# Kernel tuning notes

Measured on AMD Instinct MI355X. Metric: run time of the kernel, lower is better.

## Reference

```python
import jax, jax.numpy as jnp
import numpy as np

LN_EPS = 1e-5


def conv2d(x, w, b, stride, pad):
    # x: NCHW, w: OIHW
    y = jax.lax.conv_general_dilated(
        x, w, (stride, stride), [(pad, pad), (pad, pad)],
        dimension_numbers=("NCHW", "OIHW", "NCHW"))
    return y + b[None, :, None, None]


def gdn(x, gamma, beta):
    # y_c = x_c / sqrt(beta_c + sum_j gamma_cj * x_j^2)  (1x1 conv on x^2)
    norm = jnp.einsum("bchw,dc->bdhw", x * x, gamma) + beta[None, :, None, None]
    return x / jnp.sqrt(norm)


def layernorm(x, w, b):
    mu = jnp.mean(x, axis=-1, keepdims=True)
    var = jnp.var(x, axis=-1, keepdims=True)
    return (x - mu) / jnp.sqrt(var + LN_EPS) * w + b


def setup_inputs() -> dict:
    key = jax.random.key(0)
    ks = jax.random.split(key, 16)
    r = lambda i, shape: (jax.random.normal(ks[i], shape) * 0.02).astype(jnp.float32)
    N, M, K, D = 128, 192, 192, 128
    return {
        "x_p": jax.random.normal(ks[0], (4, 16, 3, 64, 64), jnp.float32),
        "y_g": jax.random.normal(ks[1], (64, K, 32), jnp.float32),
        "conv1_w": r(2, (N, 3, 5, 5)), "conv1_b": jnp.zeros((N,), jnp.float32),
        "gamma1": (0.1 * jnp.eye(N) + 1e-3).astype(jnp.float32), "beta1": jnp.ones((N,), jnp.float32),
        "conv2_w": r(3, (N, N, 5, 5)), "conv2_b": jnp.zeros((N,), jnp.float32),
        "gamma2": (0.1 * jnp.eye(N) + 1e-3).astype(jnp.float32), "beta2": jnp.ones((N,), jnp.float32),
        "conv3_w": r(4, (M, N, 3, 3)), "conv3_b": jnp.zeros((M,), jnp.float32),
        "ln_q_w": jnp.ones((M,), jnp.float32), "ln_q_b": jnp.zeros((M,), jnp.float32),
        "ln_kv_w": jnp.ones((K,), jnp.float32), "ln_kv_b": jnp.zeros((K,), jnp.float32),
        "ln_out_w": jnp.ones((M,), jnp.float32), "ln_out_b": jnp.zeros((M,), jnp.float32),
        "Wq": r(5, (D, M)), "Wk": r(6, (D, K)), "v_w": r(7, (1, D)),
        "Wv": r(8, (M, K)), "out_w": r(9, (M, M)), "out_b": jnp.zeros((M,), jnp.float32),
    }


def reference(x_p, y_g, conv1_w, conv1_b, gamma1, beta1, conv2_w, conv2_b,
              gamma2, beta2, conv3_w, conv3_b, ln_q_w, ln_q_b, ln_kv_w, ln_kv_b,
              ln_out_w, ln_out_b, Wq, Wk, v_w, Wv, out_w, out_b):
    B, P, C, Hp, Wp = x_p.shape
    x = x_p.reshape(B * P, C, Hp, Wp)
    # local encoder: conv s2 -> GDN -> conv s2 -> GDN -> conv s1 k3
    x = gdn(conv2d(x, conv1_w, conv1_b, 2, 2), gamma1, beta1)
    x = gdn(conv2d(x, conv2_w, conv2_b, 2, 2), gamma2, beta2)
    y_local = conv2d(x, conv3_w, conv3_b, 1, 1)          # (BP, M, h, w)
    BP, M, h, w = y_local.shape
    q = y_local.reshape(BP, M, h * w).transpose(0, 2, 1)  # (BP, Tq, M)
    kv = y_g.reshape(BP, y_g.shape[1], -1).transpose(0, 2, 1)  # (BP, Tk, K)
    q = layernorm(q, ln_q_w, ln_q_b)
    kv = layernorm(kv, ln_kv_w, ln_kv_b)
    # Bahdanau additive attention
    q_proj = jnp.einsum("bqm,dm->bqd", q, Wq)            # (BP, Tq, D)
    k_proj = jnp.einsum("bkc,dc->bkd", kv, Wk)           # (BP, Tk, D)
    energy = jnp.einsum("bqkd,d->bqk",
                        jnp.tanh(q_proj[:, :, None, :] + k_proj[:, None, :, :]),
                        v_w[0])                           # (BP, Tq, Tk)
    alpha = jax.nn.softmax(energy, axis=-1)
    v_proj = jnp.einsum("bkc,mc->bkm", kv, Wv)           # (BP, Tk, M)
    context = jnp.einsum("bqk,bkm->bqm", alpha, v_proj)
    context = jnp.einsum("bqm,nm->bqn", context, out_w) + out_b
    fused = layernorm(q + context, ln_out_w, ln_out_b)
    return fused.transpose(0, 2, 1).reshape(BP, M, h, w)
```

## Files before the change

### kernel.cpp

```cpp
#include <hip/hip_runtime.h>
#include <cstddef>
#include <cstdint>


typedef __bf16 bf16x8 __attribute__((ext_vector_type(8)));
typedef float floatx4 __attribute__((ext_vector_type(4)));
typedef unsigned short ushortT;
typedef unsigned short ushort8v __attribute__((ext_vector_type(8)));

#if __has_builtin(__builtin_amdgcn_exp2f)
#define EXP2F(x) __builtin_amdgcn_exp2f(x)
#else
#define EXP2F(x) exp2f(x)
#endif
#if __has_builtin(__builtin_amdgcn_rcpf)
#define RCPF(x) __builtin_amdgcn_rcpf(x)
#else
#define RCPF(x) (1.f / (x))
#endif

__device__ __forceinline__ ushortT f2bf(float f) {
  unsigned u = __builtin_bit_cast(unsigned, f);
  unsigned r = (u + 0x7FFFu + ((u >> 16) & 1u)) >> 16;
  return (ushortT)r;
}
__device__ __forceinline__ float bf2f(ushortT u) {
  return __builtin_bit_cast(float, ((unsigned)u) << 16);
}

static constexpr size_t OFF_X2BF = 4194304;
static constexpr size_t OFF_X3BF = 9437184;
static constexpr size_t OFF_QRAW = 10485760;
static constexpr size_t OFF_WBQ  = 21299200;
static constexpr size_t OFF_WBK  = 21311488;
static constexpr size_t OFF_WBV  = 21323776;
static constexpr size_t OFF_WBO  = 21342208;
static constexpr size_t OFF_WT2  = 26079232;
static constexpr size_t OFF_WT3  = 26284032;
static constexpr size_t OFF_WC1  = 26394624;
static constexpr size_t OFF_GB1  = 26406912;
static constexpr size_t OFF_GB2  = 26415104;
static constexpr size_t OFF_KP   = 0;
static constexpr size_t OFF_VT   = 262144;

__device__ __constant__ int d_TWI2[4][9] = {{ 0, 2, 4,10,12,14,20,22,24},
                                            { 1, 3,11,13,21,23, 0, 0, 0},
                                            { 5, 7, 9,15,17,19, 0, 0, 0},
                                            { 6, 8,16,18, 0, 0, 0, 0, 0}};
__device__ __constant__ int d_NT2[4] = {9, 6, 6, 4};

__device__ void dev_convw3_v8(const float* w, ushortT* wt, int mode, int idx8,
                              int total8) {
  if (idx8 >= total8) return;
  int base = idx8 << 3;
  int om   = (base >> 3) & 63;
  int kg   = (base >> 9) & 3;
  int slab = base >> 11;
  int mt, s, tap, T;
  if (mode == 0) {
    int ph;
    if (slab < 72) ph = 0; else if (slab < 120) ph = 1;
    else if (slab < 168) ph = 2; else ph = 3;
    const int st[4] = {0, 72, 120, 168};
    const int ns[4] = {36, 24, 24, 16};
    int rel = slab - st[ph];
    mt = rel / ns[ph]; s = rel % ns[ph];
    tap = d_TWI2[ph][s >> 2]; T = 25;
  } else {
    mt = slab / 36; s = slab % 36; tap = s >> 2; T = 9;
  }
  int cc = s & 3;
  int c0 = cc * 32 + kg * 8;
  int oc = mt * 64 + om;
  const float* wp = w + (size_t)(oc * 128 + c0) * T + tap;
  ushort8v o;
  #pragma unroll
  for (int j = 0; j < 8; ++j) o[j] = f2bf(wp[(size_t)j * T]);
  *(ushort8v*)&wt[base] = o;
}

__device__ void dev_convw1_v8(const float* w, ushortT* wt, int idx8) {
  if (idx8 >= 2560) return;
  int base = idx8 << 3;
  int k0   = base & 31;
  int oc   = (base >> 5) & 127;
  int slab = base >> 12;
  int ph, i;
  if (slab < 2) { ph = 0; i = slab; } else { ph = slab - 1; i = 0; }
  int kg = k0 >> 3;
  ushort8v o;
  #pragma unroll
  for (int jj = 0; jj < 8; ++jj) {
    int tidx = i * 8 + jj;
    float val = 0.f;
    if (kg < 3 && tidx < d_NT2[ph]) {
      int tap = d_TWI2[ph][tidx];
      val = w[(size_t)(oc * 3 + kg) * 25 + tap];
    }
    o[jj] = f2bf(val);
  }
  *(ushort8v*)&wt[base] = o;
}

__device__ void dev_wcast_v8(const float* w, ushortT* wb, int total8,
                             float scale, int idx8) {
  if (idx8 >= total8) return;
  int base = idx8 << 3;
  float4 a = *(const float4*)&w[base];
  float4 c = *(const float4*)&w[base + 4];
  ushort8v o;
  o[0] = f2bf(a.x * scale); o[1] = f2bf(a.y * scale);
  o[2] = f2bf(a.z * scale); o[3] = f2bf(a.w * scale);
  o[4] = f2bf(c.x * scale); o[5] = f2bf(c.y * scale);
  o[6] = f2bf(c.z * scale); o[7] = f2bf(c.w * scale);
  *(ushort8v*)&wb[base] = o;
}

__global__ __launch_bounds__(256) void prep_kernel(
    const float* __restrict__ conv2_w, ushortT* __restrict__ wt2,
    const float* __restrict__ conv3_w, ushortT* __restrict__ wt3,
    const float* __restrict__ conv1_w, ushortT* __restrict__ wc1,
    const float* __restrict__ Wq, ushortT* __restrict__ wbq,
    const float* __restrict__ Wk, ushortT* __restrict__ wbk,
    const float* __restrict__ Wv, ushortT* __restrict__ wbv,
    const float* __restrict__ out_w, ushortT* __restrict__ wbo,
    const float* __restrict__ gamma1, ushortT* __restrict__ gb1,
    const float* __restrict__ gamma2, ushortT* __restrict__ gb2) {
  constexpr float C2LE = 2.88539008177792681f;
  int blk = blockIdx.x, tid = threadIdx.x;
  if (blk < 200)       dev_convw3_v8(conv2_w, wt2, 0, blk * 256 + tid, 51200);
  else if (blk < 308)  dev_convw3_v8(conv3_w, wt3, 1, (blk - 200) * 256 + tid, 27648);
  else if (blk < 318)  dev_convw1_v8(conv1_w, wc1, (blk - 308) * 256 + tid);
  else if (blk < 330)  dev_wcast_v8(Wq, wbq, 3072, C2LE, (blk - 318) * 256 + tid);
  else if (blk < 342)  dev_wcast_v8(Wk, wbk, 3072, C2LE, (blk - 330) * 256 + tid);
  else if (blk < 360)  dev_wcast_v8(Wv, wbv, 4608, 1.f, (blk - 342) * 256 + tid);
  else if (blk < 378)  dev_wcast_v8(out_w, wbo, 4608, 1.f, (blk - 360) * 256 + tid);
  else if (blk < 386)  dev_wcast_v8(gamma1, gb1, 2048, 1.f, (blk - 378) * 256 + tid);
  else                 dev_wcast_v8(gamma2, gb2, 2048, 1.f, (blk - 386) * 256 + tid);
}

__global__ __launch_bounds__(256, 2) void conv1_kv_kernel(
    const float* __restrict__ x, const ushortT* __restrict__ wc1,
    const float* __restrict__ bias, const ushortT* __restrict__ gb1,
    const float* __restrict__ beta1, ushortT* __restrict__ outb,
    const float* __restrict__ yg, const float* __restrict__ ln_kv_w,
    const float* __restrict__ ln_kv_b, const ushortT* __restrict__ wbk,
    const ushortT* __restrict__ wbv, float* __restrict__ kp,
    ushortT* __restrict__ vT) {
  __shared__ ushortT smem[28416];
  int tid  = threadIdx.x;
  int wave = tid >> 6;
  int lane = tid & 63;
  int ln15 = lane & 15;
  int kg   = lane >> 4;

  if (blockIdx.x >= 512) {
    int b = blockIdx.x - 512;
    float*   skvRaw = (float*)smem;
    ushortT* skv    = smem + 12416;

    const float4* yg4 = (const float4*)(yg + (size_t)b * 6144);
    for (int j = tid; j < 1536; j += 256) {
      float4 v = yg4[j];
      int c = j >> 3;
      int t4 = (j & 7) * 4;
      skvRaw[(t4 + 0) * 194 + c] = v.x;
      skvRaw[(t4 + 1) * 194 + c] = v.y;
      skvRaw[(t4 + 2) * 194 + c] = v.z;
      skvRaw[(t4 + 3) * 194 + c] = v.w;
    }
    __syncthreads();
    for (int r = wave; r < 32; r += 4) {
      const float* src = skvRaw + r * 194;
      float v0 = src[lane], v1 = src[lane + 64], v2 = src[lane + 128];
      float s = v0 + v1 + v2;
      float s2 = v0 * v0 + v1 * v1 + v2 * v2;
      #pragma unroll
      for (int off = 32; off; off >>= 1) { s += __shfl_xor(s, off); s2 += __shfl_xor(s2, off); }
      float mean = s * (1.f / 192.f);
      float var = s2 * (1.f / 192.f) - mean * mean;
      float inv = rsqrtf(var + 1e-5f);
      skv[r * 200 + lane]       = f2bf((v0 - mean) * inv * ln_kv_w[lane]       + ln_kv_b[lane]);
      skv[r * 200 + lane + 64]  = f2bf((v1 - mean) * inv * ln_kv_w[lane + 64]  + ln_kv_b[lane + 64]);
      skv[r * 200 + lane + 128] = f2bf((v2 - mean) * inv * ln_kv_w[lane + 128] + ln_kv_b[lane + 128]);
    }
    __syncthreads();
    for (int ti = wave; ti < 40; ti += 4) {
      floatx4 acc = (floatx4)0.f;
      if (ti < 16) {
        int rt = ti >> 3, ct = ti & 7;
        #pragma unroll
        for (int k0 = 0; k0 < 192; k0 += 32) {
          bf16x8 afr = *(const bf16x8*)&skv[(rt * 16 + ln15) * 200 + k0 + kg * 8];
          bf16x8 bfr = *(const bf16x8*)&wbk[((size_t)(ct * 16 + ln15)) * 192 + k0 + kg * 8];
          acc = __builtin_amdgcn_mfma_f32_16x16x32_bf16(afr, bfr, acc, 0, 0, 0);
        }
        #pragma unroll
        for (int r = 0; r < 4; ++r)
          kp[((size_t)b * 32 + rt * 16 + kg * 4 + r) * 128 + ct * 16 + ln15] = acc[r];
      } else {
        int t2 = ti - 16;
        int rt = t2 / 12, ct = t2 % 12;
        #pragma unroll
        for (int k0 = 0; k0 < 192; k0 += 32) {
          bf16x8 afr = *(const bf16x8*)&skv[(rt * 16 + ln15) * 200 + k0 + kg * 8];
          bf16x8 bfr = *(const bf16x8*)&wbv[((size_t)(ct * 16 + ln15)) * 192 + k0 + kg * 8];
          acc = __builtin_amdgcn_mfma_f32_16x16x32_bf16(afr, bfr, acc, 0, 0, 0);
        }
        #pragma unroll
        for (int r = 0; r < 4; ++r)
          vT[((size_t)b * 192 + ct * 16 + ln15) * 32 + rt * 16 + kg * 4 + r] = f2bf(acc[r]);
      }
    }
    return;
  }

  int b  = blockIdx.x >> 3;
  int yg_ = blockIdx.x & 7;
  int y0 = yg_ * 4;

  ushortT* simg = smem;
  ushortT* sA   = smem + 2816;

  for (int j = tid; j < 1408; j += 256) ((unsigned*)simg)[j] = 0u;
  __syncthreads();

  int ihBase = 2 * y0 - 2;
  const float* xb = x + (size_t)b * 3 * 4096;
  for (int j = tid; j < 576; j += 256) {
    int q = j & 15;
    int rr = j >> 4;
    int c = rr / 12, ihl = rr % 12;
    int ih = ihBase + ihl;
    if (ih >= 0 && ih < 64) {
      float4 v = *(const float4*)&xb[c * 4096 + ih * 64 + q * 4];
      int pr = ih & 1, u = ih >> 1;
      int lr = u - y0 + 1;
      int base0 = ((pr * 2 + 0) * 3 + c) * 216 + lr * 36;
      int base1 = ((pr * 2 + 1) * 3 + c) * 216 + lr * 36;
      simg[base0 + 2 * q + 1] = f2bf(v.x);
      simg[base1 + 2 * q + 1] = f2bf(v.y);
      simg[base0 + 2 * q + 2] = f2bf(v.z);
      simg[base1 + 2 * q + 2] = f2bf(v.w);
    }
  }
  for (int j = tid; j < 2560; j += 256) {
    int chunk = j & 3, row = j >> 2;
    uint4 v = *(const uint4*)&wc1[row * 32 + chunk * 8];
    *(uint4*)&sA[row * 40 + chunk * 8] = v;
  }
  __syncthreads();

  constexpr int TDR[4][9] = {{-1,-1,-1, 0, 0, 0, 1, 1, 1},
                             {-1,-1, 0, 0, 1, 1, 0, 0, 0},
                             {-1,-1,-1, 0, 0, 0, 0, 0, 0},
                             {-1,-1, 0, 0, 0, 0, 0, 0, 0}};
  constexpr int TDC[4][9] = {{-1, 0, 1,-1, 0, 1,-1, 0, 1},
                             {-1, 0,-1, 0,-1, 0, 0, 0, 0},
                             {-1, 0, 1,-1, 0, 1, 0, 0, 0},
                             {-1, 0,-1, 0, 0, 0, 0, 0, 0}};
  constexpr int NT[4]  = {9, 6, 6, 4};
  constexpr int NM[4]  = {2, 1, 1, 1};
  constexpr int SB[4]  = {0, 2, 3, 4};

  ushort8v Bf[2][5];
  #pragma unroll
  for (int ntl = 0; ntl < 2; ++ntl) {
    int ntg = wave * 2 + ntl;
    int yloc = ntg >> 1;
    int xx = (ntg & 1) * 16 + ln15;
    int lbase = (yloc + 1) * 36 + xx + 1 + kg * 216;
    #pragma unroll
    for (int ph = 0; ph < 4; ++ph) {
      int pbase = ph * 648 + lbase;
      #pragma unroll
      for (int i = 0; i < 2; ++i) {
        if (i < NM[ph]) {
          ushort8v bv;
          #pragma unroll
          for (int j = 0; j < 8; ++j) {
            int tidx = i * 8 + j;
            if (tidx >= NT[ph]) tidx = 0;
            int off = TDR[ph][tidx] * 36 + TDC[ph][tidx];
            bv[j] = simg[pbase + off];
          }
          Bf[ntl][SB[ph] + i] = bv;
        }
      }
    }
  }

  ushort4 xq[8][2];
  #pragma unroll
  for (int m = 0; m < 8; ++m) {
    bf16x8 Af[5];
    #pragma unroll
    for (int s = 0; s < 5; ++s)
      Af[s] = *(const bf16x8*)&sA[(s * 128 + m * 16 + ln15) * 40 + kg * 8];
    int oc0 = m * 16 + kg * 4;
    float4 bv = *(const float4*)&bias[oc0];
    #pragma unroll
    for (int ntl = 0; ntl < 2; ++ntl) {
      floatx4 acc = (floatx4)0.f;
      #pragma unroll
      for (int s = 0; s < 5; ++s)
        acc = __builtin_amdgcn_mfma_f32_16x16x32_bf16(
            Af[s], __builtin_bit_cast(bf16x8, Bf[ntl][s]), acc, 0, 0, 0);
      ushort4 o4 = {f2bf(acc[0] + bv.x), f2bf(acc[1] + bv.y),
                    f2bf(acc[2] + bv.z), f2bf(acc[3] + bv.w)};
      xq[m][ntl] = o4;
    }
  }
  __syncthreads();

  for (int j = tid; j < 2048; j += 256) {
    int row = j >> 4, ch = j & 15;
    *(uint4*)&smem[row * 136 + ch * 8] = *(const uint4*)&gb1[row * 128 + ch * 8];
  }
  __syncthreads();

  const int sxbase = 17408 + wave * 2176;
  #pragma unroll
  for (int q = 0; q < 2; ++q) {
    #pragma unroll
    for (int m = 0; m < 8; ++m) {
      ushort4 xv = xq[m][q];
      float f0 = bf2f(xv.x), f1 = bf2f(xv.y), f2 = bf2f(xv.z), f3 = bf2f(xv.w);
      ushort4 s4 = {f2bf(f0 * f0), f2bf(f1 * f1), f2bf(f2 * f2), f2bf(f3 * f3)};
      *(ushort4*)&smem[sxbase + ln15 * 136 + m * 16 + kg * 4] = s4;
    }
    int ntg = wave * 2 + q;
    int y = y0 + (ntg >> 1);
    int xx = (ntg & 1) * 16 + ln15;
    int ph = ((y & 1) << 1) | (xx & 1);
    size_t dstbase = (((size_t)b * 4 + ph) * 256 + (y >> 1) * 16 + (xx >> 1)) * 128;
    #pragma unroll
    for (int dt = 0; dt < 8; ++dt) {
      floatx4 acc = (floatx4)0.f;
      #pragma unroll
      for (int k0 = 0; k0 < 4; ++k0) {
        bf16x8 ga = *(const bf16x8*)&smem[(dt * 16 + ln15) * 136 + k0 * 32 + kg * 8];
        bf16x8 xbv = *(const bf16x8*)&smem[sxbase + ln15 * 136 + k0 * 32 + kg * 8];
        acc = __builtin_amdgcn_mfma_f32_16x16x32_bf16(ga, xbv, acc, 0, 0, 0);
      }
      int d0 = dt * 16 + kg * 4;
      float4 bt = *(const float4*)&beta1[d0];
      ushort4 xv = xq[dt][q];
      ushort4 o4;
      o4.x = f2bf(bf2f(xv.x) * rsqrtf(acc[0] + bt.x));
      o4.y = f2bf(bf2f(xv.y) * rsqrtf(acc[1] + bt.y));
      o4.z = f2bf(bf2f(xv.z) * rsqrtf(acc[2] + bt.z));
      o4.w = f2bf(bf2f(xv.w) * rsqrtf(acc[3] + bt.w));
      *(ushort4*)&outb[dstbase + d0] = o4;
    }
  }
}

__global__ __launch_bounds__(512, 2) void conv2_gdn_kernel(
    const ushortT* __restrict__ X, const ushortT* __restrict__ Wt,
    const float* __restrict__ bias, const ushortT* __restrict__ gb2,
    const float* __restrict__ beta2, ushortT* __restrict__ outb) {
  int b  = blockIdx.x >> 2;
  int rs = blockIdx.x & 3;
  int r0 = rs * 4;

  int tid  = threadIdx.x;
  int wave = tid >> 6;
  int lane = tid & 63;
  int ln15 = lane & 15;
  int kg   = lane >> 4;
  int wrow  = wave & 3;
  int whalf = wave >> 2;

  __shared__ ushortT smem[29376];
  ushortT* sX2 = smem;

  auto STAGE = [&](ushortT* dst, int ph) {
    const ushortT* Xb = X + (((size_t)b * 4 + ph) * 256) * 128;
    for (int idx = tid; idx < 1728; idx += 512) {
      int chunk = idx & 15;
      int pix = idx >> 4;
      int row = pix / 18, colm = pix - row * 18;
      int i = r0 - 1 + row, j = colm - 1;
      uint4 v = {0u, 0u, 0u, 0u};
      if (i >= 0 && i < 16 && j >= 0 && j < 16)
        v = *(const uint4*)(Xb + ((size_t)(i * 16 + j)) * 128 + chunk * 8);
      *(uint4*)&dst[(row * 18 + colm) * 136 + chunk * 8] = v;
    }
  };

  floatx4 acc[4];
  #pragma unroll
  for (int m = 0; m < 4; ++m) acc[m] = (floatx4)0.f;

  constexpr int NS2[4]      = {36, 24, 24, 16};
  constexpr int PHSTART2[4] = {0, 72, 120, 168};
  constexpr int TDR_2[4][9] = {{-1,-1,-1, 0, 0, 0, 1, 1, 1},
                               {-1,-1, 0, 0, 1, 1, 0, 0, 0},
                               {-1,-1,-1, 0, 0, 0, 0, 0, 0},
                               {-1,-1, 0, 0, 0, 0, 0, 0, 0}};
  constexpr int TDC_2[4][9] = {{-1, 0, 1,-1, 0, 1,-1, 0, 1},
                               {-1, 0,-1, 0,-1, 0, 0, 0, 0},
                               {-1, 0, 1,-1, 0, 1, 0, 0, 0},
                               {-1, 0,-1, 0, 0, 0, 0, 0, 0}};

  const int aoff = kg * 512 + ln15 * 8;
  uint4 apf[8][4];

  STAGE(smem, 0);
  __syncthreads();

  #pragma unroll
  for (int ph = 0; ph < 4; ++ph) {
    ushortT* cur = (ph & 1) ? (smem + 14688) : smem;
    ushortT* nxt = (ph & 1) ? smem : (smem + 14688);
    if (ph < 3) STAGE(nxt, ph + 1);

    const int NS = NS2[ph];
    const ushortT* wp0 = Wt + (size_t)(PHSTART2[ph] + whalf * NS) * 2048 + aoff;
    #pragma unroll
    for (int jj = 0; jj < 8; ++jj) {
      #pragma unroll
      for (int m = 0; m < 4; ++m)
        apf[jj][m] = *(const uint4*)(wp0 + (size_t)jj * 2048 + m * 128);
    }

    #pragma unroll
    for (int s0 = 0; s0 < NS; s0 += 8) {
      #pragma unroll
      for (int jj = 0; jj < 8; ++jj) {
        int s = s0 + jj;
        if (s < NS) {
          bf16x8 acur[4];
          #pragma unroll
          for (int m = 0; m < 4; ++m) acur[m] = __builtin_bit_cast(bf16x8, apf[jj][m]);
          int sp = s + 8;
          if (sp < NS) {
            #pragma unroll
            for (int m = 0; m < 4; ++m)
              apf[jj][m] = *(const uint4*)(wp0 + (size_t)sp * 2048 + m * 128);
          }
          int t  = s >> 2;
          int c0 = (s & 3) * 32;
          int dr = TDR_2[ph][t];
          int dc = TDC_2[ph][t];
          bf16x8 bfr = *(const bf16x8*)&cur[((wrow + dr + 1) * 18 +
                                             (ln15 + dc + 1)) * 136 + c0 + kg * 8];
          #pragma unroll
          for (int m = 0; m < 4; ++m)
            acc[m] = __builtin_amdgcn_mfma_f32_16x16x32_bf16(acur[m], bfr, acc[m], 0, 0, 0);
        }
      }
    }
    __syncthreads();
  }

  ushort4 xq2[4];
  #pragma unroll
  for (int m = 0; m < 4; ++m) {
    int mg = whalf * 64 + m * 16 + kg * 4;
    float4 bv = *(const float4*)&bias[mg];
    ushort4 o4 = {f2bf(acc[m][0] + bv.x), f2bf(acc[m][1] + bv.y),
                  f2bf(acc[m][2] + bv.z), f2bf(acc[m][3] + bv.w)};
    xq2[m] = o4;
    float f0 = bf2f(o4.x), f1 = bf2f(o4.y), f2 = bf2f(o4.z), f3 = bf2f(o4.w);
    ushort4 s4 = {f2bf(f0 * f0), f2bf(f1 * f1), f2bf(f2 * f2), f2bf(f3 * f3)};
    *(ushort4*)&sX2[(wrow * 16 + ln15) * 136 + mg] = s4;
  }
  __syncthreads();

  int p = (r0 + wrow) * 16 + ln15;
  size_t obase = ((size_t)b * 256 + p) * 128;
  #pragma unroll
  for (int dti = 0; dti < 4; ++dti) {
    int dt = whalf * 4 + dti;
    floatx4 nacc = (floatx4)0.f;
    #pragma unroll
    for (int k0 = 0; k0 < 4; ++k0) {
      bf16x8 ga = *(const bf16x8*)&gb2[(size_t)(dt * 16 + ln15) * 128 + k0 * 32 + kg * 8];
      bf16x8 xbv = *(const bf16x8*)&sX2[(wrow * 16 + ln15) * 136 + k0 * 32 + kg * 8];
      nacc = __builtin_amdgcn_mfma_f32_16x16x32_bf16(ga, xbv, nacc, 0, 0, 0);
    }
    int d0 = dt * 16 + kg * 4;
    float4 bt = *(const float4*)&beta2[d0];
    ushort4 xv = xq2[dti];
    ushort4 o4;
    o4.x = f2bf(bf2f(xv.x) * rsqrtf(nacc[0] + bt.x));
    o4.y = f2bf(bf2f(xv.y) * rsqrtf(nacc[1] + bt.y));
    o4.z = f2bf(bf2f(xv.z) * rsqrtf(nacc[2] + bt.z));
    o4.w = f2bf(bf2f(xv.w) * rsqrtf(nacc[3] + bt.w));
    *(ushort4*)&outb[obase + d0] = o4;
  }
}

__global__ __launch_bounds__(256, 2) void conv3_mfma_kernel(
    const ushortT* __restrict__ X,
    const ushortT* __restrict__ Wt,
    const float* __restrict__ bias,
    ushortT* __restrict__ outb) {
  constexpr int OC  = 192;
  constexpr int NMT = 3;

  int b   = blockIdx.x / (NMT * 4);
  int rem = blockIdx.x % (NMT * 4);
  int mt  = rem >> 2;
  int rs  = rem & 3;
  int r0  = rs * 4;

  int wave = threadIdx.x >> 6;
  int lane = threadIdx.x & 63;
  int ln15 = lane & 15;
  int kg   = lane >> 4;

  __shared__ ushortT simg[6 * 18 * 136];

  floatx4 acc[4];
  #pragma unroll
  for (int m = 0; m < 4; ++m) acc[m] = (floatx4)0.f;

  constexpr int TDR_3[9] = {-1,-1,-1, 0, 0, 0, 1, 1, 1};
  constexpr int TDC_3[9] = {-1, 0, 1,-1, 0, 1,-1, 0, 1};

  const int aoff = kg * 512 + ln15 * 8;
  uint4 apf[8][4];

  {
    const ushortT* wp0 = Wt + (size_t)(mt * 36) * 2048 + aoff;

    const ushortT* Xb = X + ((size_t)b * 256) * 128;
    for (int idx = threadIdx.x; idx < 1728; idx += 256) {
      int chunk = idx & 15;
      int pix = idx >> 4;
      int row = pix / 18, colm = pix - row * 18;
      int i = r0 - 1 + row, j = colm - 1;
      uint4 v = {0u, 0u, 0u, 0u};
      if (i >= 0 && i < 16 && j >= 0 && j < 16)
        v = *(const uint4*)(Xb + ((size_t)(i * 16 + j)) * 128 + chunk * 8);
      *(uint4*)&simg[(row * 18 + colm) * 136 + chunk * 8] = v;
    }
    #pragma unroll
    for (int jj = 0; jj < 8; ++jj) {
      #pragma unroll
      for (int m = 0; m < 4; ++m)
        apf[jj][m] = *(const uint4*)(wp0 + (size_t)jj * 2048 + m * 128);
    }
    __syncthreads();

    #pragma unroll
    for (int s0 = 0; s0 < 36; s0 += 8) {
      #pragma unroll
      for (int jj = 0; jj < 8; ++jj) {
        int s = s0 + jj;
        if (s < 36) {
          bf16x8 acur[4];
          #pragma unroll
          for (int m = 0; m < 4; ++m) acur[m] = __builtin_bit_cast(bf16x8, apf[jj][m]);
          int sp = s + 8;
          if (sp < 36) {
            #pragma unroll
            for (int m = 0; m < 4; ++m)
              apf[jj][m] = *(const uint4*)(wp0 + (size_t)sp * 2048 + m * 128);
          }
          int t  = s >> 2;
          int c0 = (s & 3) * 32;
          int lrow = wave + TDR_3[t] + 1;
          int lcol = ln15 + TDC_3[t] + 1;
          bf16x8 bfr = *(const bf16x8*)&simg[(lrow * 18 + lcol) * 136 + c0 + kg * 8];
          #pragma unroll
          for (int m = 0; m < 4; ++m)
            acc[m] = __builtin_amdgcn_mfma_f32_16x16x32_bf16(acur[m], bfr, acc[m], 0, 0, 0);
        }
      }
    }
  }

  #pragma unroll
  for (int m = 0; m < 4; ++m) {
    int mg = mt * 64 + m * 16 + kg * 4;
    float4 bv = *(const float4*)&bias[mg];
    int r = r0 + wave;
    int p = r * 16 + ln15;
    ushort4 o4 = {f2bf(acc[m][0] + bv.x), f2bf(acc[m][1] + bv.y),
                  f2bf(acc[m][2] + bv.z), f2bf(acc[m][3] + bv.w)};
    *(ushort4*)&outb[((size_t)b * 256 + p) * OC + mg] = o4;
  }
}

__global__ __launch_bounds__(256, 4) void attn_kernel(
    const ushortT* __restrict__ qrawb, const float* __restrict__ ln_q_w,
    const float* __restrict__ ln_q_b, const float* __restrict__ kp,
    const ushortT* __restrict__ vT, const ushortT* __restrict__ wbq,
    const ushortT* __restrict__ wbo, const float* __restrict__ vw,
    const float* __restrict__ out_b, const float* __restrict__ ln_out_w,
    const float* __restrict__ ln_out_b, float* __restrict__ out) {
  __shared__ ushortT smem[17284];
  ushortT* sqln = smem;
  float*   skp  = (float*)(smem + 3200);
  float*   sqpF = (float*)(smem + 11648);
  float*   se   = (float*)(smem + 15872);
  float*   swm  = (float*)(smem + 17024);
  float*   sS0  = (float*)(smem + 17280);
  ushortT* sctx = smem;
  float*   sf   = (float*)(smem + 3200);

  int b  = blockIdx.x >> 4;
  int t0 = (blockIdx.x & 15) * 16;
  int tid  = threadIdx.x;
  int wave = tid >> 6;
  int lane = tid & 63;
  int ln15 = lane & 15;
  int kg   = lane >> 4;

  {
    const float4* kp4 = (const float4*)(kp + (size_t)b * 4096);
    for (int j = tid; j < 1024; j += 256) {
      int row = j >> 5, c4 = j & 31;
      *(float4*)&skp[row * 132 + c4 * 4] = kp4[j];
    }
  }
  float qreg[4][3];
  {
    float w0 = ln_q_w[lane], w1 = ln_q_w[lane + 64], w2 = ln_q_w[lane + 128];
    float b0 = ln_q_b[lane], b1 = ln_q_b[lane + 64], b2 = ln_q_b[lane + 128];
    #pragma unroll
    for (int i = 0; i < 4; ++i) {
      int r = wave + i * 4;
      const ushortT* xr = qrawb + ((size_t)(b * 256 + t0 + r)) * 192;
      float v0 = bf2f(xr[lane]), v1 = bf2f(xr[lane + 64]), v2 = bf2f(xr[lane + 128]);
      float s = v0 + v1 + v2;
      float s2 = v0 * v0 + v1 * v1 + v2 * v2;
      #pragma unroll
      for (int off = 32; off; off >>= 1) { s += __shfl_xor(s, off); s2 += __shfl_xor(s2, off); }
      float mean = s * (1.f / 192.f);
      float var = s2 * (1.f / 192.f) - mean * mean;
      float inv = rsqrtf(var + 1e-5f);
      float q0 = (v0 - mean) * inv * w0 + b0;
      float q1 = (v1 - mean) * inv * w1 + b1;
      float q2 = (v2 - mean) * inv * w2 + b2;
      qreg[i][0] = q0; qreg[i][1] = q1; qreg[i][2] = q2;
      sqln[r * 200 + lane]       = f2bf(q0);
      sqln[r * 200 + lane + 64]  = f2bf(q1);
      sqln[r * 200 + lane + 128] = f2bf(q2);
    }
  }
  if (tid < 128) swm[tid] = -2.f * vw[tid];
  if (tid >= 128 && tid < 192) {
    int l = tid - 128;
    float s = vw[l] + vw[l + 64];
    #pragma unroll
    for (int off = 32; off; off >>= 1) s += __shfl_xor(s, off);
    if (l == 0) *sS0 = s;
  }
  __syncthreads();

  for (int ti = wave; ti < 8; ti += 4) {
    floatx4 acc = (floatx4)0.f;
    #pragma unroll
    for (int k0 = 0; k0 < 192; k0 += 32) {
      bf16x8 afr = *(const bf16x8*)&sqln[ln15 * 200 + k0 + kg * 8];
      bf16x8 bfr = *(const bf16x8*)&wbq[((size_t)(ti * 16 + ln15)) * 192 + k0 + kg * 8];
      acc = __builtin_amdgcn_mfma_f32_16x16x32_bf16(afr, bfr, acc, 0, 0, 0);
    }
    #pragma unroll
    for (int r = 0; r < 4; ++r)
      sqpF[(kg * 4 + r) * 132 + ti * 16 + ln15] = acc[r];
  }
  __syncthreads();

  {
    float S0v = *sS0;
    int qq = tid >> 4, kc = tid & 15;
    const float4* w4 = (const float4*)swm;
    const float4* q4 = (const float4*)&sqpF[qq * 132];
    const float4* ka = (const float4*)&skp[kc * 132];
    const float4* kb = (const float4*)&skp[(kc + 16) * 132];
    float acc0 = S0v, acc1 = S0v;
    #pragma unroll 8
    for (int d4 = 0; d4 < 32; ++d4) {
      float4 qv = q4[d4], k0v = ka[d4], k1v = kb[d4], wv = w4[d4];
      acc0 += wv.x * RCPF(EXP2F(qv.x + k0v.x) + 1.f);
      acc0 += wv.y * RCPF(EXP2F(qv.y + k0v.y) + 1.f);
      acc0 += wv.z * RCPF(EXP2F(qv.z + k0v.z) + 1.f);
      acc0 += wv.w * RCPF(EXP2F(qv.w + k0v.w) + 1.f);
      acc1 += wv.x * RCPF(EXP2F(qv.x + k1v.x) + 1.f);
      acc1 += wv.y * RCPF(EXP2F(qv.y + k1v.y) + 1.f);
      acc1 += wv.z * RCPF(EXP2F(qv.z + k1v.z) + 1.f);
      acc1 += wv.w * RCPF(EXP2F(qv.w + k1v.w) + 1.f);
    }
    float mx = fmaxf(acc0, acc1);
    #pragma unroll
    for (int off = 8; off; off >>= 1) mx = fmaxf(mx, __shfl_xor(mx, off));
    float e0 = __expf(acc0 - mx), e1 = __expf(acc1 - mx);
    float s = e0 + e1;
    #pragma unroll
    for (int off = 8; off; off >>= 1) s += __shfl_xor(s, off);
    float inv = 1.f / s;
    se[qq * 36 + kc]      = e0 * inv;
    se[qq * 36 + kc + 16] = e1 * inv;
  }
  __syncthreads();

  {
    float4 a0 = *(const float4*)&se[ln15 * 36 + kg * 8];
    float4 a1 = *(const float4*)&se[ln15 * 36 + kg * 8 + 4];
    ushort8v au;
    au[0] = f2bf(a0.x); au[1] = f2bf(a0.y); au[2] = f2bf(a0.z); au[3] = f2bf(a0.w);
    au[4] = f2bf(a1.x); au[5] = f2bf(a1.y); au[6] = f2bf(a1.z); au[7] = f2bf(a1.w);
    for (int ti = wave; ti < 12; ti += 4) {
      bf16x8 bfr = *(const bf16x8*)&vT[((size_t)(b * 192 + ti * 16 + ln15)) * 32 + kg * 8];
      floatx4 acc = __builtin_amdgcn_mfma_f32_16x16x32_bf16(
          __builtin_bit_cast(bf16x8, au), bfr, (floatx4)0.f, 0, 0, 0);
      #pragma unroll
      for (int r = 0; r < 4; ++r)
        sctx[(kg * 4 + r) * 200 + ti * 16 + ln15] = f2bf(acc[r]);
    }
  }
  __syncthreads();

  for (int ti = wave; ti < 12; ti += 4) {
    floatx4 acc = (floatx4)0.f;
    #pragma unroll
    for (int k0 = 0; k0 < 192; k0 += 32) {
      bf16x8 afr = *(const bf16x8*)&sctx[ln15 * 200 + k0 + kg * 8];
      bf16x8 bfr = *(const bf16x8*)&wbo[((size_t)(ti * 16 + ln15)) * 192 + k0 + kg * 8];
      acc = __builtin_amdgcn_mfma_f32_16x16x32_bf16(afr, bfr, acc, 0, 0, 0);
    }
    float bv = out_b[ti * 16 + ln15];
    #pragma unroll
    for (int r = 0; r < 4; ++r)
      sf[(kg * 4 + r) * 193 + ti * 16 + ln15] = acc[r] + bv;
  }
  __syncthreads();

  #pragma unroll
  for (int i = 0; i < 4; ++i) {
    int rr = wave + i * 4;
    float v0 = sf[rr * 193 + lane]       + qreg[i][0];
    float v1 = sf[rr * 193 + lane + 64]  + qreg[i][1];
    float v2 = sf[rr * 193 + lane + 128] + qreg[i][2];
    float t_s = v0 + v1 + v2;
    float t_s2 = v0 * v0 + v1 * v1 + v2 * v2;
    #pragma unroll
    for (int off = 32; off; off >>= 1) { t_s += __shfl_xor(t_s, off); t_s2 += __shfl_xor(t_s2, off); }
    float m2 = t_s * (1.f / 192.f);
    float var2 = t_s2 * (1.f / 192.f) - m2 * m2;
    float inv2 = rsqrtf(var2 + 1e-5f);
    sf[rr * 193 + lane]       = (v0 - m2) * inv2 * ln_out_w[lane]       + ln_out_b[lane];
    sf[rr * 193 + lane + 64]  = (v1 - m2) * inv2 * ln_out_w[lane + 64]  + ln_out_b[lane + 64];
    sf[rr * 193 + lane + 128] = (v2 - m2) * inv2 * ln_out_w[lane + 128] + ln_out_b[lane + 128];
  }
  __syncthreads();

  for (int j = tid; j < 768; j += 256) {
    int m = j >> 2, t4 = j & 3;
    float4 o4;
    o4.x = sf[(t4 * 4 + 0) * 193 + m];
    o4.y = sf[(t4 * 4 + 1) * 193 + m];
    o4.z = sf[(t4 * 4 + 2) * 193 + m];
    o4.w = sf[(t4 * 4 + 3) * 193 + m];
    *(float4*)&out[((size_t)(b * 192 + m)) * 256 + t0 + t4 * 4] = o4;
  }
}

extern "C" void kernel_launch(void* const* d_in, const int* in_sizes, int n_in,
                              void* d_out, int out_size, void* d_ws, size_t ws_size,
                              hipStream_t stream) {
  (void)in_sizes; (void)n_in; (void)out_size; (void)ws_size;
  const float* x_p     = (const float*)d_in[0];
  const float* y_g     = (const float*)d_in[1];
  const float* conv1_w = (const float*)d_in[2];
  const float* conv1_b = (const float*)d_in[3];
  const float* gamma1  = (const float*)d_in[4];
  const float* beta1   = (const float*)d_in[5];
  const float* conv2_w = (const float*)d_in[6];
  const float* conv2_b = (const float*)d_in[7];
  const float* gamma2  = (const float*)d_in[8];
  const float* beta2   = (const float*)d_in[9];
  const float* conv3_w = (const float*)d_in[10];
  const float* conv3_b = (const float*)d_in[11];
  const float* ln_q_w  = (const float*)d_in[12];
  const float* ln_q_b  = (const float*)d_in[13];
  const float* ln_kv_w = (const float*)d_in[14];
  const float* ln_kv_b = (const float*)d_in[15];
  const float* ln_out_w= (const float*)d_in[16];
  const float* ln_out_b= (const float*)d_in[17];
  const float* Wq      = (const float*)d_in[18];
  const float* Wk      = (const float*)d_in[19];
  const float* v_w     = (const float*)d_in[20];
  const float* Wv      = (const float*)d_in[21];
  const float* out_w   = (const float*)d_in[22];
  const float* out_b   = (const float*)d_in[23];
  float* out = (float*)d_out;
  float* ws  = (float*)d_ws;

  ushortT* x2bf  = (ushortT*)(ws + OFF_X2BF);
  ushortT* x3bf  = (ushortT*)(ws + OFF_X3BF);
  ushortT* qrawb = (ushortT*)(ws + OFF_QRAW);
  ushortT* wbq   = (ushortT*)(ws + OFF_WBQ);
  ushortT* wbk   = (ushortT*)(ws + OFF_WBK);
  ushortT* wbv   = (ushortT*)(ws + OFF_WBV);
  ushortT* wbo   = (ushortT*)(ws + OFF_WBO);
  ushortT* wt2   = (ushortT*)(ws + OFF_WT2);
  ushortT* wt3   = (ushortT*)(ws + OFF_WT3);
  ushortT* wc1   = (ushortT*)(ws + OFF_WC1);
  ushortT* gb1   = (ushortT*)(ws + OFF_GB1);
  ushortT* gb2   = (ushortT*)(ws + OFF_GB2);
  float*   kp    = (float*)(ws + OFF_KP);
  ushortT* vTb   = (ushortT*)(ws + OFF_VT);

  prep_kernel<<<394, 256, 0, stream>>>(conv2_w, wt2, conv3_w, wt3, conv1_w, wc1,
                                       Wq, wbq, Wk, wbk, Wv, wbv, out_w, wbo,
                                       gamma1, gb1, gamma2, gb2);
  conv1_kv_kernel<<<576, 256, 0, stream>>>(x_p, wc1, conv1_b, gb1, beta1, x2bf,
                                           y_g, ln_kv_w, ln_kv_b, wbk, wbv,
                                           kp, vTb);
  conv2_gdn_kernel<<<256, 512, 0, stream>>>(x2bf, wt2, conv2_b, gb2, beta2, x3bf);
  conv3_mfma_kernel<<<768, 256, 0, stream>>>(x3bf, wt3, conv3_b, qrawb);
  attn_kernel<<<1024, 256, 0, stream>>>(qrawb, ln_q_w, ln_q_b, kp, vTb,
                                        wbq, wbo, v_w, out_b, ln_out_w,
                                        ln_out_b, out);
}
```

Baseline: 218.7 us.

## Split conv2+GDN into smaller blocks and drop double-buffered input staging

The conv2+GDN kernel now gives each block 2 output rows instead of 4 and launches 512 blocks instead of 256. Each wave covers 32 output channels instead of 64, so the weight-prefetch registers and accumulators shrink, and the launch bound rises to 4 blocks per SM. The per-phase input image is now staged into a single shared buffer with barriers, replacing the double-buffered prefetch. This is meant to raise occupancy and parallelism, at the cost of losing staging overlap and reading the weights across more blocks.

```diff
diff --git a/kernel.cpp b/kernel.cpp
--- a/kernel.cpp
+++ b/kernel.cpp
@@ -356,42 +356,29 @@
   }
 }
 
-__global__ __launch_bounds__(512, 2) void conv2_gdn_kernel(
+__global__ __launch_bounds__(512, 4) void conv2_gdn_kernel(
     const ushortT* __restrict__ X, const ushortT* __restrict__ Wt,
     const float* __restrict__ bias, const ushortT* __restrict__ gb2,
     const float* __restrict__ beta2, ushortT* __restrict__ outb) {
-  int b  = blockIdx.x >> 2;
-  int rs = blockIdx.x & 3;
-  int r0 = rs * 4;
+  int b  = blockIdx.x >> 3;
+  int rs = blockIdx.x & 7;
+  int r0 = rs * 2;
 
   int tid  = threadIdx.x;
   int wave = tid >> 6;
   int lane = tid & 63;
   int ln15 = lane & 15;
   int kg   = lane >> 4;
-  int wrow  = wave & 3;
-  int whalf = wave >> 2;
-
-  __shared__ ushortT smem[29376];
-  ushortT* sX2 = smem;
-
-  auto STAGE = [&](ushortT* dst, int ph) {
-    const ushortT* Xb = X + (((size_t)b * 4 + ph) * 256) * 128;
-    for (int idx = tid; idx < 1728; idx += 512) {
-      int chunk = idx & 15;
-      int pix = idx >> 4;
-      int row = pix / 18, colm = pix - row * 18;
-      int i = r0 - 1 + row, j = colm - 1;
-      uint4 v = {0u, 0u, 0u, 0u};
-      if (i >= 0 && i < 16 && j >= 0 && j < 16)
-        v = *(const uint4*)(Xb + ((size_t)(i * 16 + j)) * 128 + chunk * 8);
-      *(uint4*)&dst[(row * 18 + colm) * 136 + chunk * 8] = v;
-    }
-  };
-
-  floatx4 acc[4];
-  #pragma unroll
-  for (int m = 0; m < 4; ++m) acc[m] = (floatx4)0.f;
+  int wrow = wave & 1;
+  int wq   = wave >> 1;
+
+  __shared__ ushortT smem[14144];
+  ushortT* simg = smem;
+  ushortT* sX2  = smem + 9792;
+
+  floatx4 acc[2];
+  acc[0] = (floatx4)0.f;
+  acc[1] = (floatx4)0.f;
 
   constexpr int NS2[4]      = {36, 24, 24, 16};
   constexpr int PHSTART2[4] = {0, 72, 120, 168};
@@ -404,65 +391,67 @@
                                {-1, 0, 1,-1, 0, 1, 0, 0, 0},
                                {-1, 0,-1, 0, 0, 0, 0, 0, 0}};
 
-  const int aoff = kg * 512 + ln15 * 8;
-  uint4 apf[8][4];
-
-  STAGE(smem, 0);
-  __syncthreads();
+  const int aoff = kg * 512 + ln15 * 8 + ((wq & 1) * 2) * 128;
+  uint4 apf[4][2];
 
   #pragma unroll
   for (int ph = 0; ph < 4; ++ph) {
-    ushortT* cur = (ph & 1) ? (smem + 14688) : smem;
-    ushortT* nxt = (ph & 1) ? smem : (smem + 14688);
-    if (ph < 3) STAGE(nxt, ph + 1);
-
     const int NS = NS2[ph];
-    const ushortT* wp0 = Wt + (size_t)(PHSTART2[ph] + whalf * NS) * 2048 + aoff;
-    #pragma unroll
-    for (int jj = 0; jj < 8; ++jj) {
+    const ushortT* wp0 = Wt +
+        (size_t)(PHSTART2[ph] + (wq >> 1) * NS) * 2048 + aoff;
+
+    __syncthreads();
+    const ushortT* Xb = X + (((size_t)b * 4 + ph) * 256) * 128;
+    for (int idx = tid; idx < 1152; idx += 512) {
+      int chunk = idx & 15;
+      int pix = idx >> 4;
+      int row = pix / 18, colm = pix - row * 18;
+      int i = r0 - 1 + row, j = colm - 1;
+      uint4 v = {0u, 0u, 0u, 0u};
+      if (i >= 0 && i < 16 && j >= 0 && j < 16)
+        v = *(const uint4*)(Xb + ((size_t)(i * 16 + j)) * 128 + chunk * 8);
+      *(uint4*)&simg[(row * 18 + colm) * 136 + chunk * 8] = v;
+    }
+    #pragma unroll
+    for (int jj = 0; jj < 4; ++jj) {
+      apf[jj][0] = *(const uint4*)(wp0 + (size_t)jj * 2048);
+      apf[jj][1] = *(const uint4*)(wp0 + (size_t)jj * 2048 + 128);
+    }
+    __syncthreads();
+
+    #pragma unroll
+    for (int s0 = 0; s0 < NS; s0 += 4) {
       #pragma unroll
-      for (int m = 0; m < 4; ++m)
-        apf[jj][m] = *(const uint4*)(wp0 + (size_t)jj * 2048 + m * 128);
-    }
-
-    #pragma unroll
-    for (int s0 = 0; s0 < NS; s0 += 8) {
-      #pragma unroll
-      for (int jj = 0; jj < 8; ++jj) {
+      for (int jj = 0; jj < 4; ++jj) {
         int s = s0 + jj;
         if (s < NS) {
-          bf16x8 acur[4];
-          #pragma unroll
-          for (int m = 0; m < 4; ++m) acur[m] = __builtin_bit_cast(bf16x8, apf[jj][m]);
-          int sp = s + 8;
+          bf16x8 a0 = __builtin_bit_cast(bf16x8, apf[jj][0]);
+          bf16x8 a1 = __builtin_bit_cast(bf16x8, apf[jj][1]);
+          int sp = s + 4;
           if (sp < NS) {
-            #pragma unroll
-            for (int m = 0; m < 4; ++m)
-              apf[jj][m] = *(const uint4*)(wp0 + (size_t)sp * 2048 + m * 128);
+            apf[jj][0] = *(const uint4*)(wp0 + (size_t)sp * 2048);
+            apf[jj][1] = *(const uint4*)(wp0 + (size_t)sp * 2048 + 128);
           }
           int t  = s >> 2;
           int c0 = (s & 3) * 32;
-          int dr = TDR_2[ph][t];
-          int dc = TDC_2[ph][t];
-          bf16x8 bfr = *(const bf16x8*)&cur[((wrow + dr + 1) * 18 +
-                                             (ln15 + dc + 1)) * 136 + c0 + kg * 8];
-          #pragma unroll
-          for (int m = 0; m < 4; ++m)
-            acc[m] = __builtin_amdgcn_mfma_f32_16x16x32_bf16(acur[m], bfr, acc[m], 0, 0, 0);
+          int lrow = wrow + TDR_2[ph][t] + 1;
+          int lcol = ln15 + TDC_2[ph][t] + 1;
+          bf16x8 bfr = *(const bf16x8*)&simg[(lrow * 18 + lcol) * 136 + c0 + kg * 8];
+          acc[0] = __builtin_amdgcn_mfma_f32_16x16x32_bf16(a0, bfr, acc[0], 0, 0, 0);
+          acc[1] = __builtin_amdgcn_mfma_f32_16x16x32_bf16(a1, bfr, acc[1], 0, 0, 0);
         }
       }
     }
-    __syncthreads();
-  }
-
-  ushort4 xq2[4];
-  #pragma unroll
-  for (int m = 0; m < 4; ++m) {
-    int mg = whalf * 64 + m * 16 + kg * 4;
+  }
+
+  ushort4 xq2[2];
+  #pragma unroll
+  for (int mi = 0; mi < 2; ++mi) {
+    int mg = wq * 32 + mi * 16 + kg * 4;
     float4 bv = *(const float4*)&bias[mg];
-    ushort4 o4 = {f2bf(acc[m][0] + bv.x), f2bf(acc[m][1] + bv.y),
-                  f2bf(acc[m][2] + bv.z), f2bf(acc[m][3] + bv.w)};
-    xq2[m] = o4;
+    ushort4 o4 = {f2bf(acc[mi][0] + bv.x), f2bf(acc[mi][1] + bv.y),
+                  f2bf(acc[mi][2] + bv.z), f2bf(acc[mi][3] + bv.w)};
+    xq2[mi] = o4;
     float f0 = bf2f(o4.x), f1 = bf2f(o4.y), f2 = bf2f(o4.z), f3 = bf2f(o4.w);
     ushort4 s4 = {f2bf(f0 * f0), f2bf(f1 * f1), f2bf(f2 * f2), f2bf(f3 * f3)};
     *(ushort4*)&sX2[(wrow * 16 + ln15) * 136 + mg] = s4;
@@ -472,8 +461,8 @@
   int p = (r0 + wrow) * 16 + ln15;
   size_t obase = ((size_t)b * 256 + p) * 128;
   #pragma unroll
-  for (int dti = 0; dti < 4; ++dti) {
-    int dt = whalf * 4 + dti;
+  for (int dti = 0; dti < 2; ++dti) {
+    int dt = wq * 2 + dti;
     floatx4 nacc = (floatx4)0.f;
     #pragma unroll
     for (int k0 = 0; k0 < 4; ++k0) {
@@ -814,7 +803,7 @@
   conv1_kv_kernel<<<576, 256, 0, stream>>>(x_p, wc1, conv1_b, gb1, beta1, x2bf,
                                            y_g, ln_kv_w, ln_kv_b, wbk, wbv,
                                            kp, vTb);
-  conv2_gdn_kernel<<<256, 512, 0, stream>>>(x2bf, wt2, conv2_b, gb2, beta2, x3bf);
+  conv2_gdn_kernel<<<512, 512, 0, stream>>>(x2bf, wt2, conv2_b, gb2, beta2, x3bf);
   conv3_mfma_kernel<<<768, 256, 0, stream>>>(x3bf, wt3, conv3_b, qrawb);
   attn_kernel<<<1024, 256, 0, stream>>>(qrawb, ln_q_w, ln_q_b, kp, vTb,
                                         wbq, wbo, v_w, out_b, ln_out_w,
```

New measurement: 218.4 us. No clear change (-0.1%).
